# Kernel tuning notes

Measured on AMD Instinct MI355X. Metric: run time of the kernel, lower is better.

## Reference

```python
import jax, jax.numpy as jnp
import numpy as np

B, T, N = 2, 512, 512
H = 64          # hidden_dim
S = 8           # static_dim
C = 8           # coord_dim
DYN = 4         # dynamic feature dim (hard-coded in module)
SELF_LOOP_W = 1.0


def setup_inputs() -> dict:
    key = jax.random.key(0)
    ks = jax.random.split(key, 12)
    x = jax.random.normal(ks[0], (B, T, N), dtype=jnp.float32)
    mask = jax.random.randint(ks[1], (B, T, N), 0, 2).astype(jnp.float32)
    static_context = jax.random.normal(ks[2], (N, S), dtype=jnp.float32)
    node_coords = jax.random.normal(ks[3], (N, C), dtype=jnp.float32)
    sc = 0.1
    W1 = jax.random.normal(ks[4], (DYN + S, H), dtype=jnp.float32) * sc
    b1 = jnp.zeros((H,), dtype=jnp.float32)
    W2 = jax.random.normal(ks[5], (H, H), dtype=jnp.float32) * sc
    b2 = jnp.zeros((H,), dtype=jnp.float32)
    W3 = jax.random.normal(ks[6], (4 * H, H), dtype=jnp.float32) * sc
    b3 = jnp.zeros((H,), dtype=jnp.float32)
    W4 = jax.random.normal(ks[7], (H, 1), dtype=jnp.float32) * sc
    b4 = jnp.zeros((1,), dtype=jnp.float32)
    return {"x": x, "mask": mask, "static_context": static_context,
            "node_coords": node_coords, "W1": W1, "b1": b1, "W2": W2,
            "b2": b2, "W3": W3, "b3": b3, "W4": W4, "b4": b4}


def _dynamic_context(x, mask):
    observed = 1.0 - mask                                  # (B,T,N)
    count = jnp.maximum(observed.sum(axis=1), 1.0)          # (B,N)
    mean = (x * observed).sum(axis=1) / count               # (B,N)
    centered = (x - mean[:, None, :]) * observed
    std = jnp.sqrt((centered ** 2).sum(axis=1) / count + 1e-6)
    # last observed value per node
    t_idx = jnp.arange(x.shape[1], dtype=x.dtype)[None, :, None]
    latest = jnp.argmax(t_idx * observed, axis=1)           # (B,N) int
    last = jnp.take_along_axis(x, latest[:, None, :], axis=1)[:, 0, :]
    missing_ratio = mask.mean(axis=1)                       # (B,N)
    return jnp.stack([mean, std, last, missing_ratio], axis=-1)  # (B,N,4)


def _prior_adjacency(node_coords):
    diff = node_coords[:, None, :] - node_coords[None, :, :]  # (N,N,C)
    d2 = (diff ** 2).sum(-1)
    dist = jnp.where(d2 > 0, jnp.sqrt(jnp.where(d2 > 0, d2, 1.0)), 0.0)
    prior = 1.0 / (1.0 + dist)
    eye = jnp.eye(node_coords.shape[0], dtype=node_coords.dtype)
    return prior * (1.0 - eye)


def reference(x, mask, static_context, node_coords, W1, b1, W2, b2, W3, b3, W4, b4):
    batch = x.shape[0]
    node_dynamic = _dynamic_context(x, mask)                         # (B,N,4)
    node_static = jnp.broadcast_to(static_context[None], (batch,) + static_context.shape)
    feats = jnp.concatenate([node_dynamic, node_static], axis=-1)    # (B,N,4+S)
    h = jax.nn.relu(feats @ W1 + b1)
    node_repr = jax.nn.relu(h @ W2 + b2)                              # (B,N,H)

    h_i = node_repr[:, :, None, :]                                    # (B,N,1,H)
    h_j = node_repr[:, None, :, :]                                    # (B,1,N,H)
    hi = jnp.broadcast_to(h_i, (batch, N, N, H))
    hj = jnp.broadcast_to(h_j, (batch, N, N, H))
    pair = jnp.concatenate([hi, hj, jnp.abs(hi - hj), hi * hj], axis=-1)  # (B,N,N,4H)
    e = jax.nn.relu(pair @ W3 + b3)
    edge_mod = jax.nn.relu((e @ W4 + b4)[..., 0])                     # (B,N,N)

    prior = _prior_adjacency(node_coords)[None]                       # (1,N,N)
    eye = jnp.eye(N, dtype=x.dtype)[None]
    adapt = edge_mod * prior + eye * SELF_LOOP_W
    degree = jnp.maximum(adapt.sum(axis=-1), 1e-6)                    # (B,N)
    inv_sqrt = degree ** -0.5
    return inv_sqrt[:, :, None] * adapt * inv_sqrt[:, None, :]
```

## Files before the change

### kernel.cpp

```cpp
#include <hip/hip_runtime.h>
#include <math.h>

#define B_ 2
#define T_ 512
#define N_ 512
#define H_ 64

typedef _Float16 half8 __attribute__((ext_vector_type(8)));
typedef __attribute__((ext_vector_type(4))) float floatx4;

__device__ inline half8 habs8(half8 v) {
    union { half8 h; unsigned u[4]; } x; x.h = v;
    x.u[0] &= 0x7fff7fffu; x.u[1] &= 0x7fff7fffu;
    x.u[2] &= 0x7fff7fffu; x.u[3] &= 0x7fff7fffu;
    return x.h;
}

__global__ void prep_kernel(const float* __restrict__ x, const float* __restrict__ mask,
                            const float* __restrict__ W3,
                            float* __restrict__ part, _Float16* __restrict__ W3ph) {
    int blk = blockIdx.x;
    if (blk < 512) {
        int b  = blk >> 8;
        int nc = (blk >> 5) & 7;
        int tc = blk & 31;
        int tn = threadIdx.x & 63;
        int tt = threadIdx.x >> 6;
        int n  = nc * 64 + tn;

        float sx = 0.f, sxx = 0.f, cnt = 0.f, msum = 0.f, bv = 0.f, bt = -1.f;
#pragma unroll
        for (int it = 0; it < 4; it++) {
            int t = tc * 16 + it * 4 + tt;
            int off = (b * T_ + t) * N_ + n;
            float xv = x[off];
            float mv = mask[off];
            float obs = 1.f - mv;
            sx   += xv * obs;
            sxx  += xv * xv * obs;
            cnt  += obs;
            msum += mv;
            if (obs > 0.5f) { bt = (float)t; bv = xv; }
        }

        __shared__ float red[6][4][64];
        red[0][tt][tn] = sx;  red[1][tt][tn] = sxx; red[2][tt][tn] = cnt;
        red[3][tt][tn] = msum; red[4][tt][tn] = bv; red[5][tt][tn] = bt;
        __syncthreads();

        if (threadIdx.x < 64) {
            float Sx = 0.f, Sxx = 0.f, Cnt = 0.f, Ms = 0.f, Bv = 0.f, Bt = -1.f;
#pragma unroll
            for (int u = 0; u < 4; u++) {
                Sx  += red[0][u][tn];
                Sxx += red[1][u][tn];
                Cnt += red[2][u][tn];
                Ms  += red[3][u][tn];
                float btu = red[5][u][tn];
                if (btu > Bt) { Bt = btu; Bv = red[4][u][tn]; }
            }
            const int plane = B_ * 32 * N_;
            int base = (b * 32 + tc) * N_ + n;
            part[0 * plane + base] = Sx;
            part[1 * plane + base] = Sxx;
            part[2 * plane + base] = Cnt;
            part[3 * plane + base] = Ms;
            part[4 * plane + base] = Bv;
            part[5 * plane + base] = Bt;
        }
    } else {
        int k = (blk - 512) * 256 + threadIdx.x;
        int t = k & 7;
        int l = (k >> 3) & 63;
        int f = k >> 9;
        int s = f >> 2, nt = f & 3;
        int quad = l >> 4, col = l & 15;
        W3ph[k] = (_Float16)W3[(128 + s * 32 + quad * 8 + t) * H_ + nt * 16 + col];
    }
}

__global__ __launch_bounds__(64) void node_kernel(
        const float* __restrict__ part, const float* __restrict__ x,
        const float* __restrict__ sc,
        const float* __restrict__ W1, const float* __restrict__ b1,
        const float* __restrict__ W2, const float* __restrict__ b2,
        const float* __restrict__ W3,
        _Float16* __restrict__ nrh, float* __restrict__ P, float* __restrict__ Qp) {
    int blk = blockIdx.x;
    int b = blk >> 9;
    int n = blk & (N_ - 1);
    int o = threadIdx.x;

    __shared__ float f[12];
    __shared__ float h[H_];
    __shared__ float r[H_];

    {
        const int plane = B_ * 32 * N_;
        float Sx = 0.f, Sxx = 0.f, Cnt = 0.f, Ms = 0.f, Bv = 0.f, Bt = -1.f;
        if (o < 32) {
            int base = (b * 32 + o) * N_ + n;
            Sx  = part[0 * plane + base];
            Sxx = part[1 * plane + base];
            Cnt = part[2 * plane + base];
            Ms  = part[3 * plane + base];
            Bv  = part[4 * plane + base];
            Bt  = part[5 * plane + base];
        }
#pragma unroll
        for (int off = 1; off < 32; off <<= 1) {
            Sx  += __shfl_xor(Sx, off);
            Sxx += __shfl_xor(Sxx, off);
            Cnt += __shfl_xor(Cnt, off);
            Ms  += __shfl_xor(Ms, off);
            float obt = __shfl_xor(Bt, off);
            float obv = __shfl_xor(Bv, off);
            if (obt > Bt) { Bt = obt; Bv = obv; }
        }
        if (o == 0) {
            float count = fmaxf(Cnt, 1.f);
            float mean  = Sx / count;
            float var   = (Sxx - 2.f * mean * Sx + mean * mean * Cnt) / count;
            float stdv  = sqrtf(fmaxf(var, 0.f) + 1e-6f);
            float last  = (Bt >= 0.f) ? Bv : x[b * T_ * N_ + n];
            f[0] = mean; f[1] = stdv; f[2] = last; f[3] = Ms * (1.f / (float)T_);
        }
        if (o >= 4 && o < 12) f[o] = sc[n * 8 + (o - 4)];
    }
    __syncthreads();

    float a = b1[o];
#pragma unroll
    for (int k = 0; k < 12; k++) a += f[k] * W1[k * H_ + o];
    h[o] = fmaxf(a, 0.f);
    __syncthreads();

    float a2 = b2[o];
#pragma unroll 8
    for (int k = 0; k < H_; k++) a2 += h[k] * W2[k * H_ + o];
    float rv = fmaxf(a2, 0.f);
    r[o] = rv;
    nrh[(b * N_ + n) * H_ + o] = (_Float16)rv;
    __syncthreads();

    float p = 0.f, q = 0.f;
#pragma unroll 8
    for (int k = 0; k < H_; k++) {
        float rk = r[k];
        p += rk * W3[k * H_ + o];
        q += rk * W3[(H_ + k) * H_ + o];
    }
    P[(b * N_ + n) * H_ + o] = p;
    Qp[(b * N_ + n) * H_ + (o & 15) * 4 + (o >> 4)] = q;
}

__global__ __launch_bounds__(256) void pair_mfma_kernel(
        const _Float16* __restrict__ nrh, const float* __restrict__ P,
        const float* __restrict__ Qp, const _Float16* __restrict__ W3ph,
        const float* __restrict__ coords,
        const float* __restrict__ b3, const float* __restrict__ W4,
        const float* __restrict__ b4,
        float* __restrict__ adapt, float* __restrict__ degree) {
    int blk = blockIdx.x;
    int rb = blk >> 8;
    int ih = blk & 255;
    int i0 = ih * 2;
    int i1 = i0 + 1;
    int tid = threadIdx.x;
    int w = tid >> 6;
    int l = tid & 63;
    int col = l & 15;
    int quad = l >> 4;

    __shared__ __align__(16) float sPrior[2][N_];
    __shared__ float sRow[2][4];

#pragma unroll
    for (int s = 0; s < 2; s++) {
        int isel = i0 + s;
        float ci[8];
#pragma unroll
        for (int c = 0; c < 8; c++) ci[c] = coords[isel * 8 + c];
        for (int jj = tid; jj < N_; jj += 256) {
            float d2 = 0.f;
#pragma unroll
            for (int c = 0; c < 8; c++) {
                float df = ci[c] - coords[jj * 8 + c];
                d2 += df * df;
            }
            float dist = (d2 > 0.f) ? sqrtf(d2) : 0.f;
            sPrior[s][jj] = (jj == isel) ? 0.f : 1.f / (1.f + dist);
        }
    }

    half8 bf[4][4];
#pragma unroll
    for (int s = 0; s < 4; s++)
#pragma unroll
        for (int nt = 0; nt < 4; nt++)
            bf[s][nt] = *(const half8*)(W3ph + (((s * 4 + nt) * 64 + l) << 3));

    const _Float16* hi0_row = nrh + (rb * N_ + i0) * H_;
    const _Float16* hi1_row = nrh + (rb * N_ + i1) * H_;
    half8 hi0A = *(const half8*)(hi0_row + quad * 8);
    half8 hi0B = *(const half8*)(hi0_row + 32 + quad * 8);
    half8 hi1A = *(const half8*)(hi1_row + quad * 8);
    half8 hi1B = *(const half8*)(hi1_row + 32 + quad * 8);

    float pb30[4], pb31[4], w4v[4];
#pragma unroll
    for (int nt = 0; nt < 4; nt++) {
        int o = nt * 16 + col;
        float b3o = b3[o];
        pb30[nt] = P[(rb * N_ + i0) * H_ + o] + b3o;
        pb31[nt] = P[(rb * N_ + i1) * H_ + o] + b3o;
        w4v[nt] = W4[o];
    }
    float b4s = b4[0];
    const _Float16* nrb = nrh + (rb * N_) * H_;
    float rsum0 = 0.f, rsum1 = 0.f;
    __syncthreads();

    half8 hA, hB;
    {
        const _Float16* p0 = nrb + (w * 128 + col) * H_;
        hA = *(const half8*)(p0 + quad * 8);
        hB = *(const half8*)(p0 + 32 + quad * 8);
    }

#pragma unroll
    for (int mt = 0; mt < 8; mt++) {
        int j0 = w * 128 + mt * 16;

        half8 nA, nB;
        if (mt < 7) {
            const _Float16* pn = nrb + (j0 + 16 + col) * H_;
            nA = *(const half8*)(pn + quad * 8);
            nB = *(const half8*)(pn + 32 + quad * 8);
        }

        floatx4 pv0 = *(const floatx4*)(&sPrior[0][j0 + quad * 4]);
        floatx4 pv1 = *(const floatx4*)(&sPrior[1][j0 + quad * 4]);
        floatx4 qv[4];
#pragma unroll
        for (int r = 0; r < 4; r++)
            qv[r] = *(const floatx4*)(Qp + (rb * N_ + j0 + quad * 4 + r) * H_ + col * 4);

        {
            half8 dA = habs8(hi0A - hA);
            half8 dB = habs8(hi0B - hB);
            half8 mA = hi0A * hA;
            half8 mB = hi0B * hB;

            floatx4 acc[4];
#pragma unroll
            for (int nt = 0; nt < 4; nt++) acc[nt] = (floatx4){0.f, 0.f, 0.f, 0.f};
#pragma unroll
            for (int nt = 0; nt < 4; nt++) {
                acc[nt] = __builtin_amdgcn_mfma_f32_16x16x32_f16(dA, bf[0][nt], acc[nt], 0, 0, 0);
                acc[nt] = __builtin_amdgcn_mfma_f32_16x16x32_f16(dB, bf[1][nt], acc[nt], 0, 0, 0);
                acc[nt] = __builtin_amdgcn_mfma_f32_16x16x32_f16(mA, bf[2][nt], acc[nt], 0, 0, 0);
                acc[nt] = __builtin_amdgcn_mfma_f32_16x16x32_f16(mB, bf[3][nt], acc[nt], 0, 0, 0);
            }

            float ed[4];
#pragma unroll
            for (int r = 0; r < 4; r++) {
                int j = j0 + quad * 4 + r;
                float p = 0.f;
#pragma unroll
                for (int nt = 0; nt < 4; nt++)
                    p += fmaxf(acc[nt][r] + pb30[nt] + qv[r][nt], 0.f) * w4v[nt];
                p += __shfl_xor(p, 1);
                p += __shfl_xor(p, 2);
                p += __shfl_xor(p, 4);
                p += __shfl_xor(p, 8);
                float edge = fmaxf(p + b4s, 0.f);
                float ad = (j == i0) ? 1.0f : edge * pv0[r];
                ed[r] = ad;
                rsum0 += ad;
            }
            if (col == 0) {
                *(floatx4*)&adapt[(size_t)(rb * N_ + i0) * N_ + j0 + quad * 4] =
                    (floatx4){ed[0], ed[1], ed[2], ed[3]};
            }
        }

        {
            half8 dA = habs8(hi1A - hA);
            half8 dB = habs8(hi1B - hB);
            half8 mA = hi1A * hA;
            half8 mB = hi1B * hB;

            floatx4 acc[4];
#pragma unroll
            for (int nt = 0; nt < 4; nt++) acc[nt] = (floatx4){0.f, 0.f, 0.f, 0.f};
#pragma unroll
            for (int nt = 0; nt < 4; nt++) {
                acc[nt] = __builtin_amdgcn_mfma_f32_16x16x32_f16(dA, bf[0][nt], acc[nt], 0, 0, 0);
                acc[nt] = __builtin_amdgcn_mfma_f32_16x16x32_f16(dB, bf[1][nt], acc[nt], 0, 0, 0);
                acc[nt] = __builtin_amdgcn_mfma_f32_16x16x32_f16(mA, bf[2][nt], acc[nt], 0, 0, 0);
                acc[nt] = __builtin_amdgcn_mfma_f32_16x16x32_f16(mB, bf[3][nt], acc[nt], 0, 0, 0);
            }

            float ed[4];
#pragma unroll
            for (int r = 0; r < 4; r++) {
                int j = j0 + quad * 4 + r;
                float p = 0.f;
#pragma unroll
                for (int nt = 0; nt < 4; nt++)
                    p += fmaxf(acc[nt][r] + pb31[nt] + qv[r][nt], 0.f) * w4v[nt];
                p += __shfl_xor(p, 1);
                p += __shfl_xor(p, 2);
                p += __shfl_xor(p, 4);
                p += __shfl_xor(p, 8);
                float edge = fmaxf(p + b4s, 0.f);
                float ad = (j == i1) ? 1.0f : edge * pv1[r];
                ed[r] = ad;
                rsum1 += ad;
            }
            if (col == 0) {
                *(floatx4*)&adapt[(size_t)(rb * N_ + i1) * N_ + j0 + quad * 4] =
                    (floatx4){ed[0], ed[1], ed[2], ed[3]};
            }
        }

        if (mt < 7) { hA = nA; hB = nB; }
    }

    rsum0 += __shfl_xor(rsum0, 16);
    rsum0 += __shfl_xor(rsum0, 32);
    rsum1 += __shfl_xor(rsum1, 16);
    rsum1 += __shfl_xor(rsum1, 32);
    if (l == 0) { sRow[0][w] = rsum0; sRow[1][w] = rsum1; }
    __syncthreads();
    if (tid < 2)
        degree[rb * N_ + i0 + tid] = sRow[tid][0] + sRow[tid][1] + sRow[tid][2] + sRow[tid][3];
}

__global__ void norm_kernel(const float* __restrict__ adapt, const float* __restrict__ deg,
                            float* __restrict__ out) {
    int idx = blockIdx.x * 256 + threadIdx.x;
    int b = idx >> 16;
    int r = (idx >> 7) & (N_ - 1);
    int c4 = (idx & 127) << 2;
    float dr = rsqrtf(fmaxf(deg[b * N_ + r], 1e-6f));
    floatx4 a = *(const floatx4*)(adapt + ((size_t)idx << 2));
    floatx4 o;
#pragma unroll
    for (int k = 0; k < 4; k++)
        o[k] = dr * a[k] * rsqrtf(fmaxf(deg[b * N_ + c4 + k], 1e-6f));
    *(floatx4*)(out + ((size_t)idx << 2)) = o;
}

extern "C" void kernel_launch(void* const* d_in, const int* in_sizes, int n_in,
                              void* d_out, int out_size, void* d_ws, size_t ws_size,
                              hipStream_t stream) {
    const float* x      = (const float*)d_in[0];
    const float* mask   = (const float*)d_in[1];
    const float* sc     = (const float*)d_in[2];
    const float* coords = (const float*)d_in[3];
    const float* W1 = (const float*)d_in[4];
    const float* b1 = (const float*)d_in[5];
    const float* W2 = (const float*)d_in[6];
    const float* b2 = (const float*)d_in[7];
    const float* W3 = (const float*)d_in[8];
    const float* b3 = (const float*)d_in[9];
    const float* W4 = (const float*)d_in[10];
    const float* b4 = (const float*)d_in[11];
    float* out = (float*)d_out;

    float* wsp = (float*)d_ws;
    float* P       = wsp;
    float* Qp      = wsp + 65536;
    _Float16* nrh  = (_Float16*)(wsp + 131072);
    _Float16* W3ph = (_Float16*)(wsp + 163840);
    float* deg     = wsp + 167936;
    float* adapt   = wsp + 168960;
    float* part    = adapt;

    prep_kernel<<<544, 256, 0, stream>>>(x, mask, W3, part, W3ph);
    node_kernel<<<B_ * N_, 64, 0, stream>>>(part, x, sc, W1, b1, W2, b2, W3, nrh, P, Qp);
    pair_mfma_kernel<<<512, 256, 0, stream>>>(nrh, P, Qp, W3ph, coords, b3, W4, b4, adapt, deg);
    norm_kernel<<<512, 256, 0, stream>>>(adapt, deg, out);
}
```

Baseline: 109.5 us.

## Fuse node, pair and norm kernels into one persistent kernel with grid barriers

Merges the node MLP, pairwise MFMA edge kernel and normalization kernel into a single 512-block kernel that uses atomic-counter grid barriers between phases, and folds the W3 fp16 repack into the stats prep kernel. The goal is to cut kernel launch overhead and inter-kernel gaps. The cost is that node work runs on only half the threads of each block, and the spin barriers assume all 512 blocks are co-resident. If they are not, the barrier times out and correctness fails. The 'part' buffer is moved so it no longer aliases adapt.

Result: slower. 200.0 us (+82.7%).

```diff
diff --git a/kernel.cpp b/kernel.cpp
--- a/kernel.cpp
+++ b/kernel.cpp
@@ -5,6 +5,7 @@
 #define T_ 512
 #define N_ 512
 #define H_ 64
+#define NBLK 512u
 
 typedef _Float16 half8 __attribute__((ext_vector_type(8)));
 typedef __attribute__((ext_vector_type(4))) float floatx4;
@@ -16,60 +17,76 @@
     return x.h;
 }
 
+__device__ inline void grid_barrier(unsigned* cnt) {
+    __syncthreads();
+    if (threadIdx.x == 0) {
+        __threadfence();
+        __hip_atomic_fetch_add(cnt, 1u, __ATOMIC_ACQ_REL, __HIP_MEMORY_SCOPE_AGENT);
+        unsigned spins = 0;
+        while (__hip_atomic_load(cnt, __ATOMIC_ACQUIRE, __HIP_MEMORY_SCOPE_AGENT) < NBLK) {
+            __builtin_amdgcn_s_sleep(2);
+            if (++spins > (1u << 20)) break;
+        }
+        __threadfence();
+    }
+    __syncthreads();
+}
+
 __global__ void prep_kernel(const float* __restrict__ x, const float* __restrict__ mask,
                             const float* __restrict__ W3,
-                            float* __restrict__ part, _Float16* __restrict__ W3ph) {
+                            float* __restrict__ part, _Float16* __restrict__ W3ph,
+                            unsigned* __restrict__ cnt) {
     int blk = blockIdx.x;
-    if (blk < 512) {
-        int b  = blk >> 8;
-        int nc = (blk >> 5) & 7;
-        int tc = blk & 31;
-        int tn = threadIdx.x & 63;
-        int tt = threadIdx.x >> 6;
-        int n  = nc * 64 + tn;
-
-        float sx = 0.f, sxx = 0.f, cnt = 0.f, msum = 0.f, bv = 0.f, bt = -1.f;
-#pragma unroll
-        for (int it = 0; it < 4; it++) {
-            int t = tc * 16 + it * 4 + tt;
-            int off = (b * T_ + t) * N_ + n;
-            float xv = x[off];
-            float mv = mask[off];
-            float obs = 1.f - mv;
-            sx   += xv * obs;
-            sxx  += xv * xv * obs;
-            cnt  += obs;
-            msum += mv;
-            if (obs > 0.5f) { bt = (float)t; bv = xv; }
-        }
-
-        __shared__ float red[6][4][64];
-        red[0][tt][tn] = sx;  red[1][tt][tn] = sxx; red[2][tt][tn] = cnt;
-        red[3][tt][tn] = msum; red[4][tt][tn] = bv; red[5][tt][tn] = bt;
-        __syncthreads();
-
-        if (threadIdx.x < 64) {
-            float Sx = 0.f, Sxx = 0.f, Cnt = 0.f, Ms = 0.f, Bv = 0.f, Bt = -1.f;
-#pragma unroll
-            for (int u = 0; u < 4; u++) {
-                Sx  += red[0][u][tn];
-                Sxx += red[1][u][tn];
-                Cnt += red[2][u][tn];
-                Ms  += red[3][u][tn];
-                float btu = red[5][u][tn];
-                if (btu > Bt) { Bt = btu; Bv = red[4][u][tn]; }
-            }
-            const int plane = B_ * 32 * N_;
-            int base = (b * 32 + tc) * N_ + n;
-            part[0 * plane + base] = Sx;
-            part[1 * plane + base] = Sxx;
-            part[2 * plane + base] = Cnt;
-            part[3 * plane + base] = Ms;
-            part[4 * plane + base] = Bv;
-            part[5 * plane + base] = Bt;
-        }
-    } else {
-        int k = (blk - 512) * 256 + threadIdx.x;
+    int b  = blk >> 8;
+    int nc = (blk >> 5) & 7;
+    int tc = blk & 31;
+    int tn = threadIdx.x & 63;
+    int tt = threadIdx.x >> 6;
+    int n  = nc * 64 + tn;
+
+    float sx = 0.f, sxx = 0.f, cnt_ = 0.f, msum = 0.f, bv = 0.f, bt = -1.f;
+#pragma unroll
+    for (int it = 0; it < 4; it++) {
+        int t = tc * 16 + it * 4 + tt;
+        int off = (b * T_ + t) * N_ + n;
+        float xv = x[off];
+        float mv = mask[off];
+        float obs = 1.f - mv;
+        sx   += xv * obs;
+        sxx  += xv * xv * obs;
+        cnt_ += obs;
+        msum += mv;
+        if (obs > 0.5f) { bt = (float)t; bv = xv; }
+    }
+
+    __shared__ float red[6][4][64];
+    red[0][tt][tn] = sx;  red[1][tt][tn] = sxx; red[2][tt][tn] = cnt_;
+    red[3][tt][tn] = msum; red[4][tt][tn] = bv; red[5][tt][tn] = bt;
+    __syncthreads();
+
+    if (threadIdx.x < 64) {
+        float Sx = 0.f, Sxx = 0.f, Cnt = 0.f, Ms = 0.f, Bv = 0.f, Bt = -1.f;
+#pragma unroll
+        for (int u = 0; u < 4; u++) {
+            Sx  += red[0][u][tn];
+            Sxx += red[1][u][tn];
+            Cnt += red[2][u][tn];
+            Ms  += red[3][u][tn];
+            float btu = red[5][u][tn];
+            if (btu > Bt) { Bt = btu; Bv = red[4][u][tn]; }
+        }
+        const int plane = B_ * 32 * N_;
+        int base = (b * 32 + tc) * N_ + n;
+        part[0 * plane + base] = Sx;
+        part[1 * plane + base] = Sxx;
+        part[2 * plane + base] = Cnt;
+        part[3 * plane + base] = Ms;
+        part[4 * plane + base] = Bv;
+        part[5 * plane + base] = Bt;
+    }
+
+    if (blk < 32) {
+        int k = blk * 256 + threadIdx.x;
         int t = k & 7;
         int l = (k >> 3) & 63;
         int f = k >> 9;
@@ -77,281 +94,294 @@
         int quad = l >> 4, col = l & 15;
         W3ph[k] = (_Float16)W3[(128 + s * 32 + quad * 8 + t) * H_ + nt * 16 + col];
     }
+    if (blk == 0 && threadIdx.x < 2) cnt[threadIdx.x] = 0u;
 }
 
-__global__ __launch_bounds__(64) void node_kernel(
+__global__ __launch_bounds__(256, 2) void mega_kernel(
         const float* __restrict__ part, const float* __restrict__ x,
         const float* __restrict__ sc,
         const float* __restrict__ W1, const float* __restrict__ b1,
         const float* __restrict__ W2, const float* __restrict__ b2,
-        const float* __restrict__ W3,
-        _Float16* __restrict__ nrh, float* __restrict__ P, float* __restrict__ Qp) {
-    int blk = blockIdx.x;
-    int b = blk >> 9;
-    int n = blk & (N_ - 1);
-    int o = threadIdx.x;
-
-    __shared__ float f[12];
-    __shared__ float h[H_];
-    __shared__ float r[H_];
+        const float* __restrict__ W3, const float* __restrict__ b3,
+        const float* __restrict__ W4, const float* __restrict__ b4,
+        const float* __restrict__ coords, const _Float16* __restrict__ W3ph,
+        _Float16* __restrict__ nrh, float* __restrict__ P, float* __restrict__ Qp,
+        float* __restrict__ adapt, float* __restrict__ degree,
+        float* __restrict__ out, unsigned* __restrict__ cnt) {
+    int tid = threadIdx.x;
+
+    __shared__ union SMem {
+        struct { float f[2][12]; float h[2][64]; float r[2][64]; } nb;
+        struct { __align__(16) float sPrior[2][N_]; float sRow[2][4]; } pr;
+    } sm;
 
     {
-        const int plane = B_ * 32 * N_;
-        float Sx = 0.f, Sxx = 0.f, Cnt = 0.f, Ms = 0.f, Bv = 0.f, Bt = -1.f;
-        if (o < 32) {
-            int base = (b * 32 + o) * N_ + n;
-            Sx  = part[0 * plane + base];
-            Sxx = part[1 * plane + base];
-            Cnt = part[2 * plane + base];
-            Ms  = part[3 * plane + base];
-            Bv  = part[4 * plane + base];
-            Bt  = part[5 * plane + base];
-        }
-#pragma unroll
-        for (int off = 1; off < 32; off <<= 1) {
-            Sx  += __shfl_xor(Sx, off);
-            Sxx += __shfl_xor(Sxx, off);
-            Cnt += __shfl_xor(Cnt, off);
-            Ms  += __shfl_xor(Ms, off);
-            float obt = __shfl_xor(Bt, off);
-            float obv = __shfl_xor(Bv, off);
-            if (obt > Bt) { Bt = obt; Bv = obv; }
-        }
-        if (o == 0) {
-            float count = fmaxf(Cnt, 1.f);
-            float mean  = Sx / count;
-            float var   = (Sxx - 2.f * mean * Sx + mean * mean * Cnt) / count;
-            float stdv  = sqrtf(fmaxf(var, 0.f) + 1e-6f);
-            float last  = (Bt >= 0.f) ? Bv : x[b * T_ * N_ + n];
-            f[0] = mean; f[1] = stdv; f[2] = last; f[3] = Ms * (1.f / (float)T_);
-        }
-        if (o >= 4 && o < 12) f[o] = sc[n * 8 + (o - 4)];
-    }
-    __syncthreads();
-
-    float a = b1[o];
-#pragma unroll
-    for (int k = 0; k < 12; k++) a += f[k] * W1[k * H_ + o];
-    h[o] = fmaxf(a, 0.f);
-    __syncthreads();
-
-    float a2 = b2[o];
+        int g = tid >> 6;
+        int o = tid & 63;
+        bool act = (g < 2);
+        int gg = g & 1;
+        int task = blockIdx.x * 2 + gg;
+        int b = (task >> 9) & 1;
+        int n = task & (N_ - 1);
+
+        if (act) {
+            const int plane = B_ * 32 * N_;
+            float Sx = 0.f, Sxx = 0.f, Cnt = 0.f, Ms = 0.f, Bv = 0.f, Bt = -1.f;
+            if (o < 32) {
+                int base = (b * 32 + o) * N_ + n;
+                Sx  = part[0 * plane + base];
+                Sxx = part[1 * plane + base];
+                Cnt = part[2 * plane + base];
+                Ms  = part[3 * plane + base];
+                Bv  = part[4 * plane + base];
+                Bt  = part[5 * plane + base];
+            }
+#pragma unroll
+            for (int off = 1; off < 32; off <<= 1) {
+                Sx  += __shfl_xor(Sx, off);
+                Sxx += __shfl_xor(Sxx, off);
+                Cnt += __shfl_xor(Cnt, off);
+                Ms  += __shfl_xor(Ms, off);
+                float obt = __shfl_xor(Bt, off);
+                float obv = __shfl_xor(Bv, off);
+                if (obt > Bt) { Bt = obt; Bv = obv; }
+            }
+            if (o == 0) {
+                float count = fmaxf(Cnt, 1.f);
+                float mean  = Sx / count;
+                float var   = (Sxx - 2.f * mean * Sx + mean * mean * Cnt) / count;
+                float stdv  = sqrtf(fmaxf(var, 0.f) + 1e-6f);
+                float last  = (Bt >= 0.f) ? Bv : x[b * T_ * N_ + n];
+                sm.nb.f[gg][0] = mean; sm.nb.f[gg][1] = stdv;
+                sm.nb.f[gg][2] = last; sm.nb.f[gg][3] = Ms * (1.f / (float)T_);
+            }
+            if (o >= 4 && o < 12) sm.nb.f[gg][o] = sc[n * 8 + (o - 4)];
+        }
+        __syncthreads();
+
+        if (act) {
+            float a = b1[o];
+#pragma unroll
+            for (int k = 0; k < 12; k++) a += sm.nb.f[gg][k] * W1[k * H_ + o];
+            sm.nb.h[gg][o] = fmaxf(a, 0.f);
+        }
+        __syncthreads();
+
+        if (act) {
+            float a2 = b2[o];
 #pragma unroll 8
-    for (int k = 0; k < H_; k++) a2 += h[k] * W2[k * H_ + o];
-    float rv = fmaxf(a2, 0.f);
-    r[o] = rv;
-    nrh[(b * N_ + n) * H_ + o] = (_Float16)rv;
-    __syncthreads();
-
-    float p = 0.f, q = 0.f;
+            for (int k = 0; k < H_; k++) a2 += sm.nb.h[gg][k] * W2[k * H_ + o];
+            float rv = fmaxf(a2, 0.f);
+            sm.nb.r[gg][o] = rv;
+            nrh[(b * N_ + n) * H_ + o] = (_Float16)rv;
+        }
+        __syncthreads();
+
+        if (act) {
+            float p = 0.f, q = 0.f;
 #pragma unroll 8
-    for (int k = 0; k < H_; k++) {
-        float rk = r[k];
-        p += rk * W3[k * H_ + o];
-        q += rk * W3[(H_ + k) * H_ + o];
-    }
-    P[(b * N_ + n) * H_ + o] = p;
-    Qp[(b * N_ + n) * H_ + (o & 15) * 4 + (o >> 4)] = q;
-}
-
-__global__ __launch_bounds__(256) void pair_mfma_kernel(
-        const _Float16* __restrict__ nrh, const float* __restrict__ P,
-        const float* __restrict__ Qp, const _Float16* __restrict__ W3ph,
-        const float* __restrict__ coords,
-        const float* __restrict__ b3, const float* __restrict__ W4,
-        const float* __restrict__ b4,
-        float* __restrict__ adapt, float* __restrict__ degree) {
-    int blk = blockIdx.x;
-    int rb = blk >> 8;
-    int ih = blk & 255;
-    int i0 = ih * 2;
-    int i1 = i0 + 1;
-    int tid = threadIdx.x;
-    int w = tid >> 6;
-    int l = tid & 63;
-    int col = l & 15;
-    int quad = l >> 4;
-
-    __shared__ __align__(16) float sPrior[2][N_];
-    __shared__ float sRow[2][4];
-
-#pragma unroll
-    for (int s = 0; s < 2; s++) {
-        int isel = i0 + s;
-        float ci[8];
-#pragma unroll
-        for (int c = 0; c < 8; c++) ci[c] = coords[isel * 8 + c];
-        for (int jj = tid; jj < N_; jj += 256) {
-            float d2 = 0.f;
-#pragma unroll
-            for (int c = 0; c < 8; c++) {
-                float df = ci[c] - coords[jj * 8 + c];
-                d2 += df * df;
-            }
-            float dist = (d2 > 0.f) ? sqrtf(d2) : 0.f;
-            sPrior[s][jj] = (jj == isel) ? 0.f : 1.f / (1.f + dist);
-        }
-    }
-
-    half8 bf[4][4];
-#pragma unroll
-    for (int s = 0; s < 4; s++)
-#pragma unroll
-        for (int nt = 0; nt < 4; nt++)
-            bf[s][nt] = *(const half8*)(W3ph + (((s * 4 + nt) * 64 + l) << 3));
-
-    const _Float16* hi0_row = nrh + (rb * N_ + i0) * H_;
-    const _Float16* hi1_row = nrh + (rb * N_ + i1) * H_;
-    half8 hi0A = *(const half8*)(hi0_row + quad * 8);
-    half8 hi0B = *(const half8*)(hi0_row + 32 + quad * 8);
-    half8 hi1A = *(const half8*)(hi1_row + quad * 8);
-    half8 hi1B = *(const half8*)(hi1_row + 32 + quad * 8);
-
-    float pb30[4], pb31[4], w4v[4];
-#pragma unroll
-    for (int nt = 0; nt < 4; nt++) {
-        int o = nt * 16 + col;
-        float b3o = b3[o];
-        pb30[nt] = P[(rb * N_ + i0) * H_ + o] + b3o;
-        pb31[nt] = P[(rb * N_ + i1) * H_ + o] + b3o;
-        w4v[nt] = W4[o];
-    }
-    float b4s = b4[0];
-    const _Float16* nrb = nrh + (rb * N_) * H_;
-    float rsum0 = 0.f, rsum1 = 0.f;
-    __syncthreads();
-
-    half8 hA, hB;
+            for (int k = 0; k < H_; k++) {
+                float rk = sm.nb.r[gg][k];
+                p += rk * W3[k * H_ + o];
+                q += rk * W3[(H_ + k) * H_ + o];
+            }
+            P[(b * N_ + n) * H_ + o] = p;
+            Qp[(b * N_ + n) * H_ + (o & 15) * 4 + (o >> 4)] = q;
+        }
+    }
+
+    grid_barrier(&cnt[0]);
+
     {
-        const _Float16* p0 = nrb + (w * 128 + col) * H_;
-        hA = *(const half8*)(p0 + quad * 8);
-        hB = *(const half8*)(p0 + 32 + quad * 8);
-    }
-
-#pragma unroll
-    for (int mt = 0; mt < 8; mt++) {
-        int j0 = w * 128 + mt * 16;
-
-        half8 nA, nB;
-        if (mt < 7) {
-            const _Float16* pn = nrb + (j0 + 16 + col) * H_;
-            nA = *(const half8*)(pn + quad * 8);
-            nB = *(const half8*)(pn + 32 + quad * 8);
-        }
-
-        floatx4 pv0 = *(const floatx4*)(&sPrior[0][j0 + quad * 4]);
-        floatx4 pv1 = *(const floatx4*)(&sPrior[1][j0 + quad * 4]);
-        floatx4 qv[4];
-#pragma unroll
-        for (int r = 0; r < 4; r++)
-            qv[r] = *(const floatx4*)(Qp + (rb * N_ + j0 + quad * 4 + r) * H_ + col * 4);
-
+        int blk = blockIdx.x;
+        int rb = blk >> 8;
+        int ih = blk & 255;
+        int i0 = ih * 2;
+        int i1 = i0 + 1;
+        int w = tid >> 6;
+        int l = tid & 63;
+        int col = l & 15;
+        int quad = l >> 4;
+
+#pragma unroll
+        for (int s = 0; s < 2; s++) {
+            int isel = i0 + s;
+            float ci[8];
+#pragma unroll
+            for (int c = 0; c < 8; c++) ci[c] = coords[isel * 8 + c];
+            for (int jj = tid; jj < N_; jj += 256) {
+                float d2 = 0.f;
+#pragma unroll
+                for (int c = 0; c < 8; c++) {
+                    float df = ci[c] - coords[jj * 8 + c];
+                    d2 += df * df;
+                }
+                float dist = (d2 > 0.f) ? sqrtf(d2) : 0.f;
+                sm.pr.sPrior[s][jj] = (jj == isel) ? 0.f : 1.f / (1.f + dist);
+            }
+        }
+
+        half8 bf[4][4];
+#pragma unroll
+        for (int s = 0; s < 4; s++)
+#pragma unroll
+            for (int nt = 0; nt < 4; nt++)
+                bf[s][nt] = *(const half8*)(W3ph + (((s * 4 + nt) * 64 + l) << 3));
+
+        const _Float16* hi0_row = nrh + (rb * N_ + i0) * H_;
+        const _Float16* hi1_row = nrh + (rb * N_ + i1) * H_;
+        half8 hi0A = *(const half8*)(hi0_row + quad * 8);
+        half8 hi0B = *(const half8*)(hi0_row + 32 + quad * 8);
+        half8 hi1A = *(const half8*)(hi1_row + quad * 8);
+        half8 hi1B = *(const half8*)(hi1_row + 32 + quad * 8);
+
+        float pb30[4], pb31[4], w4v[4];
+#pragma unroll
+        for (int nt = 0; nt < 4; nt++) {
+            int o = nt * 16 + col;
+            float b3o = b3[o];
+            pb30[nt] = P[(rb * N_ + i0) * H_ + o] + b3o;
+            pb31[nt] = P[(rb * N_ + i1) * H_ + o] + b3o;
+            w4v[nt] = W4[o];
+        }
+        float b4s = b4[0];
+        const _Float16* nrb = nrh + (rb * N_) * H_;
+        float rsum0 = 0.f, rsum1 = 0.f;
+        __syncthreads();
+
+        half8 hA, hB;
         {
-            half8 dA = habs8(hi0A - hA);
-            half8 dB = habs8(hi0B - hB);
-            half8 mA = hi0A * hA;
-            half8 mB = hi0B * hB;
-
-            floatx4 acc[4];
-#pragma unroll
-            for (int nt = 0; nt < 4; nt++) acc[nt] = (floatx4){0.f, 0.f, 0.f, 0.f};
-#pragma unroll
-            for (int nt = 0; nt < 4; nt++) {
-                acc[nt] = __builtin_amdgcn_mfma_f32_16x16x32_f16(dA, bf[0][nt], acc[nt], 0, 0, 0);
-                acc[nt] = __builtin_amdgcn_mfma_f32_16x16x32_f16(dB, bf[1][nt], acc[nt], 0, 0, 0);
-                acc[nt] = __builtin_amdgcn_mfma_f32_16x16x32_f16(mA, bf[2][nt], acc[nt], 0, 0, 0);
-                acc[nt] = __builtin_amdgcn_mfma_f32_16x16x32_f16(mB, bf[3][nt], acc[nt], 0, 0, 0);
-            }
-
-            float ed[4];
-#pragma unroll
-            for (int r = 0; r < 4; r++) {
-                int j = j0 + quad * 4 + r;
-                float p = 0.f;
-#pragma unroll
-                for (int nt = 0; nt < 4; nt++)
-                    p += fmaxf(acc[nt][r] + pb30[nt] + qv[r][nt], 0.f) * w4v[nt];
-                p += __shfl_xor(p, 1);
-                p += __shfl_xor(p, 2);
-                p += __shfl_xor(p, 4);
-                p += __shfl_xor(p, 8);
-                float edge = fmaxf(p + b4s, 0.f);
-                float ad = (j == i0) ? 1.0f : edge * pv0[r];
-                ed[r] = ad;
-                rsum0 += ad;
-            }
-            if (col == 0) {
-                *(floatx4*)&adapt[(size_t)(rb * N_ + i0) * N_ + j0 + quad * 4] =
-                    (floatx4){ed[0], ed[1], ed[2], ed[3]};
-            }
-        }
-
-        {
-            half8 dA = habs8(hi1A - hA);
-            half8 dB = habs8(hi1B - hB);
-            half8 mA = hi1A * hA;
-            half8 mB = hi1B * hB;
-
-            floatx4 acc[4];
-#pragma unroll
-            for (int nt = 0; nt < 4; nt++) acc[nt] = (floatx4){0.f, 0.f, 0.f, 0.f};
-#pragma unroll
-            for (int nt = 0; nt < 4; nt++) {
-                acc[nt] = __builtin_amdgcn_mfma_f32_16x16x32_f16(dA, bf[0][nt], acc[nt], 0, 0, 0);
-                acc[nt] = __builtin_amdgcn_mfma_f32_16x16x32_f16(dB, bf[1][nt], acc[nt], 0, 0, 0);
-                acc[nt] = __builtin_amdgcn_mfma_f32_16x16x32_f16(mA, bf[2][nt], acc[nt], 0, 0, 0);
-                acc[nt] = __builtin_amdgcn_mfma_f32_16x16x32_f16(mB, bf[3][nt], acc[nt], 0, 0, 0);
-            }
-
-            float ed[4];
-#pragma unroll
-            for (int r = 0; r < 4; r++) {
-                int j = j0 + quad * 4 + r;
-                float p = 0.f;
-#pragma unroll
-                for (int nt = 0; nt < 4; nt++)
-                    p += fmaxf(acc[nt][r] + pb31[nt] + qv[r][nt], 0.f) * w4v[nt];
-                p += __shfl_xor(p, 1);
-                p += __shfl_xor(p, 2);
-                p += __shfl_xor(p, 4);
-                p += __shfl_xor(p, 8);
-                float edge = fmaxf(p + b4s, 0.f);
-                float ad = (j == i1) ? 1.0f : edge * pv1[r];
-                ed[r] = ad;
-                rsum1 += ad;
-            }
-            if (col == 0) {
-                *(floatx4*)&adapt[(size_t)(rb * N_ + i1) * N_ + j0 + quad * 4] =
-                    (floatx4){ed[0], ed[1], ed[2], ed[3]};
-            }
-        }
-
-        if (mt < 7) { hA = nA; hB = nB; }
-    }
-
-    rsum0 += __shfl_xor(rsum0, 16);
-    rsum0 += __shfl_xor(rsum0, 32);
-    rsum1 += __shfl_xor(rsum1, 16);
-    rsum1 += __shfl_xor(rsum1, 32);
-    if (l == 0) { sRow[0][w] = rsum0; sRow[1][w] = rsum1; }
-    __syncthreads();
-    if (tid < 2)
-        degree[rb * N_ + i0 + tid] = sRow[tid][0] + sRow[tid][1] + sRow[tid][2] + sRow[tid][3];
-}
-
-__global__ void norm_kernel(const float* __restrict__ adapt, const float* __restrict__ deg,
-                            float* __restrict__ out) {
-    int idx = blockIdx.x * 256 + threadIdx.x;
-    int b = idx >> 16;
-    int r = (idx >> 7) & (N_ - 1);
-    int c4 = (idx & 127) << 2;
-    float dr = rsqrtf(fmaxf(deg[b * N_ + r], 1e-6f));
-    floatx4 a = *(const floatx4*)(adapt + ((size_t)idx << 2));
-    floatx4 o;
-#pragma unroll
-    for (int k = 0; k < 4; k++)
-        o[k] = dr * a[k] * rsqrtf(fmaxf(deg[b * N_ + c4 + k], 1e-6f));
-    *(floatx4*)(out + ((size_t)idx << 2)) = o;
+            const _Float16* p0 = nrb + (w * 128 + col) * H_;
+            hA = *(const half8*)(p0 + quad * 8);
+            hB = *(const half8*)(p0 + 32 + quad * 8);
+        }
+
+#pragma unroll
+        for (int mt = 0; mt < 8; mt++) {
+            int j0 = w * 128 + mt * 16;
+
+            half8 nA, nB;
+            if (mt < 7) {
+                const _Float16* pn = nrb + (j0 + 16 + col) * H_;
+                nA = *(const half8*)(pn + quad * 8);
+                nB = *(const half8*)(pn + 32 + quad * 8);
+            }
+
+            floatx4 pv0 = *(const floatx4*)(&sm.pr.sPrior[0][j0 + quad * 4]);
+            floatx4 pv1 = *(const floatx4*)(&sm.pr.sPrior[1][j0 + quad * 4]);
+            floatx4 qv[4];
+#pragma unroll
+            for (int r = 0; r < 4; r++)
+                qv[r] = *(const floatx4*)(Qp + (rb * N_ + j0 + quad * 4 + r) * H_ + col * 4);
+
+            {
+                half8 dA = habs8(hi0A - hA);
+                half8 dB = habs8(hi0B - hB);
+                half8 mA = hi0A * hA;
+                half8 mB = hi0B * hB;
+
+                floatx4 acc[4];
+#pragma unroll
+                for (int nt = 0; nt < 4; nt++) acc[nt] = (floatx4){0.f, 0.f, 0.f, 0.f};
+#pragma unroll
+                for (int nt = 0; nt < 4; nt++) {
+                    acc[nt] = __builtin_amdgcn_mfma_f32_16x16x32_f16(dA, bf[0][nt], acc[nt], 0, 0, 0);
+                    acc[nt] = __builtin_amdgcn_mfma_f32_16x16x32_f16(dB, bf[1][nt], acc[nt], 0, 0, 0);
+                    acc[nt] = __builtin_amdgcn_mfma_f32_16x16x32_f16(mA, bf[2][nt], acc[nt], 0, 0, 0);
+                    acc[nt] = __builtin_amdgcn_mfma_f32_16x16x32_f16(mB, bf[3][nt], acc[nt], 0, 0, 0);
+                }
+
+                float ed[4];
+#pragma unroll
+                for (int r = 0; r < 4; r++) {
+                    int j = j0 + quad * 4 + r;
+                    float p = 0.f;
+#pragma unroll
+                    for (int nt = 0; nt < 4; nt++)
+                        p += fmaxf(acc[nt][r] + pb30[nt] + qv[r][nt], 0.f) * w4v[nt];
+                    p += __shfl_xor(p, 1);
+                    p += __shfl_xor(p, 2);
+                    p += __shfl_xor(p, 4);
+                    p += __shfl_xor(p, 8);
+                    float edge = fmaxf(p + b4s, 0.f);
+                    float ad = (j == i0) ? 1.0f : edge * pv0[r];
+                    ed[r] = ad;
+                    rsum0 += ad;
+                }
+                if (col == 0) {
+                    *(floatx4*)&adapt[(size_t)(rb * N_ + i0) * N_ + j0 + quad * 4] =
+                        (floatx4){ed[0], ed[1], ed[2], ed[3]};
+                }
+            }
+
+            {
+                half8 dA = habs8(hi1A - hA);
+                half8 dB = habs8(hi1B - hB);
+                half8 mA = hi1A * hA;
+                half8 mB = hi1B * hB;
+
+                floatx4 acc[4];
+#pragma unroll
+                for (int nt = 0; nt < 4; nt++) acc[nt] = (floatx4){0.f, 0.f, 0.f, 0.f};
+#pragma unroll
+                for (int nt = 0; nt < 4; nt++) {
+                    acc[nt] = __builtin_amdgcn_mfma_f32_16x16x32_f16(dA, bf[0][nt], acc[nt], 0, 0, 0);
+                    acc[nt] = __builtin_amdgcn_mfma_f32_16x16x32_f16(dB, bf[1][nt], acc[nt], 0, 0, 0);
+                    acc[nt] = __builtin_amdgcn_mfma_f32_16x16x32_f16(mA, bf[2][nt], acc[nt], 0, 0, 0);
+                    acc[nt] = __builtin_amdgcn_mfma_f32_16x16x32_f16(mB, bf[3][nt], acc[nt], 0, 0, 0);
+                }
+
+                float ed[4];
+#pragma unroll
+                for (int r = 0; r < 4; r++) {
+                    int j = j0 + quad * 4 + r;
+                    float p = 0.f;
+#pragma unroll
+                    for (int nt = 0; nt < 4; nt++)
+                        p += fmaxf(acc[nt][r] + pb31[nt] + qv[r][nt], 0.f) * w4v[nt];
+                    p += __shfl_xor(p, 1);
+                    p += __shfl_xor(p, 2);
+                    p += __shfl_xor(p, 4);
+                    p += __shfl_xor(p, 8);
+                    float edge = fmaxf(p + b4s, 0.f);
+                    float ad = (j == i1) ? 1.0f : edge * pv1[r];
+                    ed[r] = ad;
+                    rsum1 += ad;
+                }
+                if (col == 0) {
+                    *(floatx4*)&adapt[(size_t)(rb * N_ + i1) * N_ + j0 + quad * 4] =
+                        (floatx4){ed[0], ed[1], ed[2], ed[3]};
+                }
+            }
+
+            if (mt < 7) { hA = nA; hB = nB; }
+        }
+
+        rsum0 += __shfl_xor(rsum0, 16);
+        rsum0 += __shfl_xor(rsum0, 32);
+        rsum1 += __shfl_xor(rsum1, 16);
+        rsum1 += __shfl_xor(rsum1, 32);
+        if (l == 0) { sm.pr.sRow[0][w] = rsum0; sm.pr.sRow[1][w] = rsum1; }
+        __syncthreads();
+        if (tid < 2)
+            degree[rb * N_ + i0 + tid] =
+                sm.pr.sRow[tid][0] + sm.pr.sRow[tid][1] + sm.pr.sRow[tid][2] + sm.pr.sRow[tid][3];
+    }
+
+    grid_barrier(&cnt[1]);
+
+    {
+        int idx = blockIdx.x * 256 + tid;
+        int b = idx >> 16;
+        int c4 = (idx & 127) << 2;
+        float dr = rsqrtf(fmaxf(degree[b * N_ + ((idx >> 7) & (N_ - 1))], 1e-6f));
+        floatx4 a = *(const floatx4*)(adapt + ((size_t)idx << 2));
+        floatx4 o;
+#pragma unroll
+        for (int k = 0; k < 4; k++)
+            o[k] = dr * a[k] * rsqrtf(fmaxf(degree[b * N_ + c4 + k], 1e-6f));
+        *(floatx4*)(out + ((size_t)idx << 2)) = o;
+    }
 }
 
 extern "C" void kernel_launch(void* const* d_in, const int* in_sizes, int n_in,
@@ -377,11 +407,11 @@
     _Float16* nrh  = (_Float16*)(wsp + 131072);
     _Float16* W3ph = (_Float16*)(wsp + 163840);
     float* deg     = wsp + 167936;
-    float* adapt   = wsp + 168960;
-    float* part    = adapt;
-
-    prep_kernel<<<544, 256, 0, stream>>>(x, mask, W3, part, W3ph);
-    node_kernel<<<B_ * N_, 64, 0, stream>>>(part, x, sc, W1, b1, W2, b2, W3, nrh, P, Qp);
-    pair_mfma_kernel<<<512, 256, 0, stream>>>(nrh, P, Qp, W3ph, coords, b3, W4, b4, adapt, deg);
-    norm_kernel<<<512, 256, 0, stream>>>(adapt, deg, out);
+    unsigned* cnt  = (unsigned*)(wsp + 168960);
+    float* adapt   = wsp + 169024;
+    float* part    = wsp + 693312;
+
+    prep_kernel<<<512, 256, 0, stream>>>(x, mask, W3, part, W3ph, cnt);
+    mega_kernel<<<512, 256, 0, stream>>>(part, x, sc, W1, b1, W2, b2, W3, b3, W4, b4,
+                                         coords, W3ph, nrh, P, Qp, adapt, deg, out, cnt);
 }
```
